# Kernel optimization log

Measured on AMD Instinct MI355X. Metric: run time of the kernel, lower is better.

## Reference

```python
import jax, jax.numpy as jnp
import numpy as np

TOP_K = 2  # MoE top-k routing


def setup_inputs() -> dict:
    key = jax.random.key(0)
    ks = jax.random.split(key, 5)
    B, D, H, O, N = 8192, 3072, 128, 10, 8
    scale_g = 1.0 / np.sqrt(D)
    return {
        "x": jax.random.normal(ks[0], (B, D), dtype=jnp.float32),
        "Wg": jax.random.normal(ks[1], (D, N), dtype=jnp.float32) * scale_g,
        "bg": jnp.zeros((N,), dtype=jnp.float32),
        "W1": jax.random.normal(ks[2], (N, D, H), dtype=jnp.float32) * scale_g,
        "b1": jnp.zeros((N, H), dtype=jnp.float32),
        "W2": jax.random.normal(ks[3], (N, H, O), dtype=jnp.float32) * (1.0 / np.sqrt(H)),
        "b2": jnp.zeros((N, O), dtype=jnp.float32),
    }


def reference(x, Wg, bg, W1, b1, W2, b2):
    # Gating: logits -> top-k -> softmax over the k selected logits
    g = x @ Wg + bg                                  # [B, N]
    tv, ti = jax.lax.top_k(g, TOP_K)                 # [B, k]
    w = jax.nn.softmax(tv, axis=-1)                  # [B, k]
    # Expert MLPs, computed densely over all experts (vectorized dispatch)
    h = jax.nn.relu(jnp.einsum('bd,edh->beh', x, W1) + b1)   # [B, N, H]
    y = jnp.einsum('beh,eho->beo', h, W2) + b2               # [B, N, O]
    # Combine: gather each token's k selected expert outputs, weight, sum
    ysel = jnp.take_along_axis(y, ti[:, :, None], axis=1)    # [B, k, O]
    return jnp.sum(w[:, :, None] * ysel, axis=1)             # [B, O]
```

## Files before the change

### kernel.cpp

```cpp
#include <hip/hip_runtime.h>
#include <hip/hip_bf16.h>

#define B_TOK 8192
#define D_DIM 3072
#define H_DIM 128
#define O_DIM 10
#define N_EXP 8

#define BM 128
#define BK2 128
#define HLDS_STRIDE 136

typedef __bf16 bf16x8 __attribute__((ext_vector_type(8)));
typedef float  f32x4  __attribute__((ext_vector_type(4)));
typedef unsigned short us8 __attribute__((ext_vector_type(8)));

__device__ __forceinline__ unsigned short f2bf(float f) {
  unsigned int u = __float_as_uint(f);
  unsigned int r = (u + 0x7FFFu + ((u >> 16) & 1u)) >> 16;
  return (unsigned short)r;
}

__device__ __forceinline__ void async16(const void* g, void* l) {
  __builtin_amdgcn_global_load_lds(
      (const __attribute__((address_space(1))) void*)g,
      (__attribute__((address_space(3))) void*)l,
      16, 0, 0);
}

__global__ __launch_bounds__(256) void k0_w1_transpose(const float* __restrict__ W1,
                                                       unsigned short* __restrict__ w1t) {
  __shared__ __align__(16) unsigned short lds[64 * 72];
  const int e  = blockIdx.z;
  const int d0 = blockIdx.x * 64;
  const int h0 = blockIdx.y * 64;
  const int tid = threadIdx.x;

  const float* src = W1 + ((size_t)e * D_DIM + d0) * H_DIM + h0;
  const int hl = tid & 63;
  const int dg = tid >> 6;
#pragma unroll
  for (int k = 0; k < 16; ++k) {
    const int d = dg + 4 * k;
    lds[hl * 72 + d] = f2bf(src[(size_t)d * H_DIM + hl]);
  }
  __syncthreads();

  unsigned short* dst = w1t + ((size_t)e * H_DIM + h0) * D_DIM + d0;
  const int q  = tid & 7;
  const int h1 = tid >> 3;
#pragma unroll
  for (int k = 0; k < 2; ++k) {
    const int h = h1 + 32 * k;
    const int d = q * 8;
    us8 v = *(const us8*)(lds + h * 72 + d);
    *(us8*)(dst + (size_t)h * D_DIM + d) = v;
  }
}

__global__ __launch_bounds__(512) void k1_gate_convert(
    const float* __restrict__ x, const float* __restrict__ Wg,
    const float* __restrict__ bg, unsigned short* __restrict__ xb,
    int4* __restrict__ idx4, float2* __restrict__ wts, int* __restrict__ cnt) {
  __shared__ float wg_lds[N_EXP * D_DIM];
  __shared__ int lcnt[N_EXP], gbase[N_EXP];
  const int tid = threadIdx.x;

  if (tid < N_EXP) lcnt[tid] = 0;
  for (int f = tid; f < D_DIM * N_EXP / 4; f += 512) {
    const float4 v = ((const float4*)Wg)[f];
    const int d  = f >> 1;
    const int nh = (f & 1) * 4;
    wg_lds[(nh + 0) * D_DIM + d] = v.x;
    wg_lds[(nh + 1) * D_DIM + d] = v.y;
    wg_lds[(nh + 2) * D_DIM + d] = v.z;
    wg_lds[(nh + 3) * D_DIM + d] = v.w;
  }
  __syncthreads();

  const int lane = tid & 63;
  const int wv   = tid >> 6;
  const int tk0  = blockIdx.x * 32 + wv * 4;

  const float* xr0 = x + (size_t)(tk0 + 0) * D_DIM;
  const float* xr1 = x + (size_t)(tk0 + 1) * D_DIM;
  const float* xr2 = x + (size_t)(tk0 + 2) * D_DIM;
  const float* xr3 = x + (size_t)(tk0 + 3) * D_DIM;
  unsigned short* xw0 = xb + (size_t)(tk0 + 0) * D_DIM;
  unsigned short* xw1 = xb + (size_t)(tk0 + 1) * D_DIM;
  unsigned short* xw2 = xb + (size_t)(tk0 + 2) * D_DIM;
  unsigned short* xw3 = xb + (size_t)(tk0 + 3) * D_DIM;

  float acc[4][N_EXP];
#pragma unroll
  for (int t = 0; t < 4; ++t)
#pragma unroll
    for (int n = 0; n < N_EXP; ++n) acc[t][n] = 0.f;

#pragma unroll 2
  for (int jj = 0; jj < D_DIM / 64; ++jj) {
    const int d = jj * 64 + lane;
    float w8[N_EXP];
#pragma unroll
    for (int n = 0; n < N_EXP; ++n) w8[n] = wg_lds[n * D_DIM + d];
    const float x0 = xr0[d], x1 = xr1[d], x2 = xr2[d], x3 = xr3[d];
    xw0[d] = f2bf(x0); xw1[d] = f2bf(x1); xw2[d] = f2bf(x2); xw3[d] = f2bf(x3);
#pragma unroll
    for (int n = 0; n < N_EXP; ++n) {
      acc[0][n] = fmaf(x0, w8[n], acc[0][n]);
      acc[1][n] = fmaf(x1, w8[n], acc[1][n]);
      acc[2][n] = fmaf(x2, w8[n], acc[2][n]);
      acc[3][n] = fmaf(x3, w8[n], acc[3][n]);
    }
  }

#pragma unroll
  for (int t = 0; t < 4; ++t)
#pragma unroll
    for (int n = 0; n < N_EXP; ++n) {
#pragma unroll
      for (int off = 32; off > 0; off >>= 1)
        acc[t][n] += __shfl_xor(acc[t][n], off, 64);
    }

  int li0[4], li1[4], lp0[4], lp1[4];
  float lw0[4], lw1[4];
  if (lane == 0) {
#pragma unroll
    for (int t = 0; t < 4; ++t) {
      float g[N_EXP];
#pragma unroll
      for (int n = 0; n < N_EXP; ++n) g[n] = acc[t][n] + bg[n];
      int i0 = 0;
#pragma unroll
      for (int n = 1; n < N_EXP; ++n) if (g[n] > g[i0]) i0 = n;
      int i1 = (i0 == 0) ? 1 : 0;
#pragma unroll
      for (int n = 0; n < N_EXP; ++n) if (n != i0 && g[n] > g[i1]) i1 = n;
      float e1 = expf(g[i1] - g[i0]);
      float inv = 1.f / (1.f + e1);
      li0[t] = i0; li1[t] = i1;
      lw0[t] = inv; lw1[t] = e1 * inv;
      lp0[t] = atomicAdd(&lcnt[i0], 1);
      lp1[t] = atomicAdd(&lcnt[i1], 1);
    }
  }
  __syncthreads();
  if (tid < N_EXP) gbase[tid] = atomicAdd(&cnt[tid], lcnt[tid]);
  __syncthreads();
  if (lane == 0) {
#pragma unroll
    for (int t = 0; t < 4; ++t) {
      idx4[tk0 + t] = make_int4(li0[t], gbase[li0[t]] + lp0[t],
                                li1[t], gbase[li1[t]] + lp1[t]);
      wts[tk0 + t]  = make_float2(lw0[t], lw1[t]);
    }
  }
}

__global__ void k1b1_scan(const int* __restrict__ cnt, int* __restrict__ off_g) {
  if (threadIdx.x == 0) {
    int s = 0;
#pragma unroll
    for (int n = 0; n < N_EXP; ++n) {
      off_g[n] = s;
      s += (cnt[n] + BM - 1) / BM * BM;
    }
    off_g[N_EXP] = s;
  }
}

__global__ __launch_bounds__(256) void k1b2_scatter(
    const int* __restrict__ off_g, const int4* __restrict__ idx4,
    int* __restrict__ tlist) {
  const int t = blockIdx.x * 256 + threadIdx.x;
  if (t >= B_TOK) return;
  const int4 r = idx4[t];
  tlist[off_g[r.x] + r.y] = t;
  tlist[off_g[r.z] + r.w] = t;
}

__global__ __launch_bounds__(256) void k2_experts(
    const unsigned short* __restrict__ xb,
    const unsigned short* __restrict__ w1t,
    const float* __restrict__ b1,
    const float* __restrict__ W2,
    const float* __restrict__ b2,
    const int* __restrict__ cnt, const int* __restrict__ off_g,
    const int* __restrict__ tlist,
    float* __restrict__ ypair) {
  const int e    = blockIdx.y;
  const int n_e  = cnt[e];
  const int row0 = blockIdx.x * BM;
  if (row0 >= n_e) return;
  const int off_e = off_g[e];

  __shared__ __align__(16) unsigned short sm[65536 + 2048];
  unsigned short* h_lds   = sm;
  unsigned short* w2t_lds = sm + 65536;

  const int tid  = threadIdx.x;
  const int lane = tid & 63;
  const int wv   = tid >> 6;

  const float* W2e = W2 + (size_t)e * H_DIM * O_DIM;
  for (int idx = tid; idx < 16 * 128; idx += 256) {
    int o = idx >> 7, hh = idx & 127;
    float v = (o < O_DIM) ? W2e[hh * O_DIM + o] : 0.f;
    w2t_lds[idx] = f2bf(v);
  }

  const int mhalf = (wv >> 1) * 64;
  const int nhalf = (wv & 1) * 64;

  f32x4 acc[4][4];
#pragma unroll
  for (int i = 0; i < 4; ++i)
#pragma unroll
    for (int j = 0; j < 4; ++j)
      acc[i][j] = (f32x4){0.f, 0.f, 0.f, 0.f};

  const int quad = lane >> 4;
  const int koff0 = (lane & 15) * 8;
  const unsigned short* Abase[8];
  const unsigned short* Bbase[8];
#pragma unroll
  for (int j = 0; j < 8; ++j) {
    int rloc = wv * 32 + j * 4 + quad;
    int gr = row0 + rloc;
    gr = gr < n_e ? gr : n_e - 1;
    Abase[j] = xb + (size_t)tlist[off_e + gr] * D_DIM + koff0;
    Bbase[j] = w1t + ((size_t)e * H_DIM + rloc) * D_DIM + koff0;
  }

#define STAGE(it, pp)                                                     \
  {                                                                       \
    const int ko = (it) * BK2;                                            \
    unsigned short* abuf = sm + (pp) * 32768;                             \
    unsigned short* bbuf = sm + 16384 + (pp) * 32768;                     \
    _Pragma("unroll")                                                     \
    for (int j = 0; j < 8; ++j) {                                         \
      const int ldsrow = (wv * 32 + j * 4) * BK2;                         \
      async16(Abase[j] + ko, abuf + ldsrow);                              \
      async16(Bbase[j] + ko, bbuf + ldsrow);                              \
    }                                                                     \
  }

  STAGE(0, 0);

  const int NIT = D_DIM / BK2;
  for (int it = 0; it < NIT; ++it) {
    __syncthreads();
    if (it + 1 < NIT) STAGE(it + 1, (it + 1) & 1);
    const unsigned short* al = sm + (it & 1) * 32768;
    const unsigned short* bl = sm + 16384 + (it & 1) * 32768;
#pragma unroll
    for (int kk = 0; kk < 4; ++kk) {
      const int krd = kk * 32 + quad * 8;
      bf16x8 af[4], bfr[4];
#pragma unroll
      for (int mi = 0; mi < 4; ++mi)
        af[mi] = *(const bf16x8*)(al + (mhalf + mi * 16 + (lane & 15)) * BK2 + krd);
#pragma unroll
      for (int ni = 0; ni < 4; ++ni)
        bfr[ni] = *(const bf16x8*)(bl + (nhalf + ni * 16 + (lane & 15)) * BK2 + krd);
#pragma unroll
      for (int mi = 0; mi < 4; ++mi)
#pragma unroll
        for (int ni = 0; ni < 4; ++ni)
          acc[mi][ni] = __builtin_amdgcn_mfma_f32_16x16x32_bf16(af[mi], bfr[ni], acc[mi][ni], 0, 0, 0);
    }
  }
  __syncthreads();

  const float* b1e = b1 + e * H_DIM;
#pragma unroll
  for (int ni = 0; ni < 4; ++ni) {
    const int col  = nhalf + ni * 16 + (lane & 15);
    const float bias = b1e[col];
#pragma unroll
    for (int mi = 0; mi < 4; ++mi) {
      const int rbase = mhalf + mi * 16 + (quad << 2);
#pragma unroll
      for (int r = 0; r < 4; ++r) {
        float v = acc[mi][ni][r] + bias;
        v = v > 0.f ? v : 0.f;
        h_lds[(rbase + r) * HLDS_STRIDE + col] = f2bf(v);
      }
    }
  }
  __syncthreads();

  f32x4 acc2[2];
  acc2[0] = (f32x4){0.f, 0.f, 0.f, 0.f};
  acc2[1] = (f32x4){0.f, 0.f, 0.f, 0.f};
#pragma unroll
  for (int ks = 0; ks < 4; ++ks) {
    const int krd = ks * 32 + quad * 8;
    bf16x8 bfr = *(const bf16x8*)(w2t_lds + (lane & 15) * 128 + krd);
#pragma unroll
    for (int mi = 0; mi < 2; ++mi) {
      bf16x8 afr = *(const bf16x8*)(h_lds + (wv * 32 + mi * 16 + (lane & 15)) * HLDS_STRIDE + krd);
      acc2[mi] = __builtin_amdgcn_mfma_f32_16x16x32_bf16(afr, bfr, acc2[mi], 0, 0, 0);
    }
  }
  const int o = lane & 15;
  if (o < O_DIM) {
    const float bias2 = b2[e * O_DIM + o];
#pragma unroll
    for (int mi = 0; mi < 2; ++mi) {
#pragma unroll
      for (int r = 0; r < 4; ++r) {
        const int rl = wv * 32 + mi * 16 + (quad << 2) + r;
        if (row0 + rl < n_e)
          ypair[(size_t)(off_e + row0 + rl) * 16 + o] = acc2[mi][r] + bias2;
      }
    }
  }
}

__global__ __launch_bounds__(256) void k3_combine(
    const float* __restrict__ ypair, const int4* __restrict__ idx4,
    const float2* __restrict__ wts, const int* __restrict__ off_g,
    float* __restrict__ out) {
  const int g = blockIdx.x * 256 + threadIdx.x;
  if (g >= B_TOK * O_DIM) return;
  const int b = g / O_DIM, o = g - b * O_DIM;
  const int4 r = idx4[b];
  const float2 w = wts[b];
  out[g] = w.x * ypair[(size_t)(off_g[r.x] + r.y) * 16 + o] +
           w.y * ypair[(size_t)(off_g[r.z] + r.w) * 16 + o];
}

extern "C" void kernel_launch(void* const* d_in, const int* in_sizes, int n_in,
                              void* d_out, int out_size, void* d_ws, size_t ws_size,
                              hipStream_t stream) {
  const float* x  = (const float*)d_in[0];
  const float* Wg = (const float*)d_in[1];
  const float* bg = (const float*)d_in[2];
  const float* W1 = (const float*)d_in[3];
  const float* b1 = (const float*)d_in[4];
  const float* W2 = (const float*)d_in[5];
  const float* b2 = (const float*)d_in[6];
  float* out = (float*)d_out;

  char* ws = (char*)d_ws;
  unsigned short* xb  = (unsigned short*)ws;
  unsigned short* w1t = (unsigned short*)(ws + 50331648);
  int4*   idx4  = (int4*)  (ws + 56623104);
  float2* wts   = (float2*)(ws + 56754176);
  int*    cnt   = (int*)   (ws + 56819712);
  int*    off_g = (int*)   (ws + 56819840);
  int*    tlist = (int*)   (ws + 56819968);
  float*  ypair = (float*) (ws + 56890112);

  k0_w1_transpose<<<dim3(48, 2, 8), dim3(256), 0, stream>>>(W1, w1t);
  (void)hipMemsetAsync(cnt, 0, N_EXP * sizeof(int), stream);
  k1_gate_convert<<<dim3(B_TOK / 32), dim3(512), 0, stream>>>(x, Wg, bg, xb, idx4, wts, cnt);
  k1b1_scan<<<dim3(1), dim3(64), 0, stream>>>(cnt, off_g);
  k1b2_scatter<<<dim3(B_TOK / 256), dim3(256), 0, stream>>>(off_g, idx4, tlist);
  k2_experts<<<dim3(B_TOK / BM, N_EXP), dim3(256), 0, stream>>>(
      xb, w1t, b1, W2, b2, cnt, off_g, tlist, ypair);
  k3_combine<<<dim3((B_TOK * O_DIM + 255) / 256), dim3(256), 0, stream>>>(
      ypair, idx4, wts, off_g, out);
}
```

Measured before the change: 270.6 us.

## Split gate GEMV over D chunks with separate top-k reduction kernel

The fused gate/convert kernel is split in two. The first kernel processes 768-wide D chunks across a 2D grid, using vectorized float4 loads of x and the gate weights, and writes per-chunk partial logits. The second kernel sums the four partials, adds the bias, and does top-2 selection, softmax and expert counting. This shrinks the LDS footprint per block and gives many more, smaller blocks, aiming for higher occupancy and bandwidth while streaming x. The cost is one extra launch and a small partial-logit buffer that aliases later workspace regions.

```diff
diff --git a/kernel.cpp b/kernel.cpp
--- a/kernel.cpp
+++ b/kernel.cpp
@@ -10,6 +10,8 @@
 #define BM 128
 #define BK2 128
 #define HLDS_STRIDE 136
+#define CHK 768
+#define NCHK 4
 
 typedef __bf16 bf16x8 __attribute__((ext_vector_type(8)));
 typedef float  f32x4  __attribute__((ext_vector_type(4)));
@@ -58,38 +60,37 @@
   }
 }
 
-__global__ __launch_bounds__(512) void k1_gate_convert(
+__global__ __launch_bounds__(256) void k1a_stream(
     const float* __restrict__ x, const float* __restrict__ Wg,
-    const float* __restrict__ bg, unsigned short* __restrict__ xb,
-    int4* __restrict__ idx4, float2* __restrict__ wts, int* __restrict__ cnt) {
-  __shared__ float wg_lds[N_EXP * D_DIM];
-  __shared__ int lcnt[N_EXP], gbase[N_EXP];
+    unsigned short* __restrict__ xb, float* __restrict__ gpart) {
+  __shared__ float wg_lds[N_EXP * CHK];
+  const int c   = blockIdx.y;
+  const int d0  = c * CHK;
   const int tid = threadIdx.x;
 
-  if (tid < N_EXP) lcnt[tid] = 0;
-  for (int f = tid; f < D_DIM * N_EXP / 4; f += 512) {
-    const float4 v = ((const float4*)Wg)[f];
-    const int d  = f >> 1;
+  for (int f = tid; f < CHK * N_EXP / 4; f += 256) {
+    const float4 v = ((const float4*)(Wg + (size_t)d0 * N_EXP))[f];
+    const int dl = f >> 1;
     const int nh = (f & 1) * 4;
-    wg_lds[(nh + 0) * D_DIM + d] = v.x;
-    wg_lds[(nh + 1) * D_DIM + d] = v.y;
-    wg_lds[(nh + 2) * D_DIM + d] = v.z;
-    wg_lds[(nh + 3) * D_DIM + d] = v.w;
+    wg_lds[(nh + 0) * CHK + dl] = v.x;
+    wg_lds[(nh + 1) * CHK + dl] = v.y;
+    wg_lds[(nh + 2) * CHK + dl] = v.z;
+    wg_lds[(nh + 3) * CHK + dl] = v.w;
   }
   __syncthreads();
 
   const int lane = tid & 63;
   const int wv   = tid >> 6;
-  const int tk0  = blockIdx.x * 32 + wv * 4;
-
-  const float* xr0 = x + (size_t)(tk0 + 0) * D_DIM;
-  const float* xr1 = x + (size_t)(tk0 + 1) * D_DIM;
-  const float* xr2 = x + (size_t)(tk0 + 2) * D_DIM;
-  const float* xr3 = x + (size_t)(tk0 + 3) * D_DIM;
-  unsigned short* xw0 = xb + (size_t)(tk0 + 0) * D_DIM;
-  unsigned short* xw1 = xb + (size_t)(tk0 + 1) * D_DIM;
-  unsigned short* xw2 = xb + (size_t)(tk0 + 2) * D_DIM;
-  unsigned short* xw3 = xb + (size_t)(tk0 + 3) * D_DIM;
+  const int t0   = blockIdx.x * 16 + wv * 4;
+
+  const float* xr0 = x + (size_t)(t0 + 0) * D_DIM + d0;
+  const float* xr1 = x + (size_t)(t0 + 1) * D_DIM + d0;
+  const float* xr2 = x + (size_t)(t0 + 2) * D_DIM + d0;
+  const float* xr3 = x + (size_t)(t0 + 3) * D_DIM + d0;
+  unsigned short* xw0 = xb + (size_t)(t0 + 0) * D_DIM + d0;
+  unsigned short* xw1 = xb + (size_t)(t0 + 1) * D_DIM + d0;
+  unsigned short* xw2 = xb + (size_t)(t0 + 2) * D_DIM + d0;
+  unsigned short* xw3 = xb + (size_t)(t0 + 3) * D_DIM + d0;
 
   float acc[4][N_EXP];
 #pragma unroll
@@ -97,20 +98,44 @@
 #pragma unroll
     for (int n = 0; n < N_EXP; ++n) acc[t][n] = 0.f;
 
-#pragma unroll 2
-  for (int jj = 0; jj < D_DIM / 64; ++jj) {
-    const int d = jj * 64 + lane;
-    float w8[N_EXP];
-#pragma unroll
-    for (int n = 0; n < N_EXP; ++n) w8[n] = wg_lds[n * D_DIM + d];
-    const float x0 = xr0[d], x1 = xr1[d], x2 = xr2[d], x3 = xr3[d];
-    xw0[d] = f2bf(x0); xw1[d] = f2bf(x1); xw2[d] = f2bf(x2); xw3[d] = f2bf(x3);
+#pragma unroll
+  for (int s = 0; s < CHK / 256; ++s) {
+    const int dl = s * 256 + lane * 4;
+    float4 xv0 = *(const float4*)(xr0 + dl);
+    float4 xv1 = *(const float4*)(xr1 + dl);
+    float4 xv2 = *(const float4*)(xr2 + dl);
+    float4 xv3 = *(const float4*)(xr3 + dl);
+    float4 w4[N_EXP];
+#pragma unroll
+    for (int n = 0; n < N_EXP; ++n)
+      w4[n] = *(const float4*)(wg_lds + n * CHK + dl);
+    ushort4 p;
+    p.x = f2bf(xv0.x); p.y = f2bf(xv0.y); p.z = f2bf(xv0.z); p.w = f2bf(xv0.w);
+    *(ushort4*)(xw0 + dl) = p;
+    p.x = f2bf(xv1.x); p.y = f2bf(xv1.y); p.z = f2bf(xv1.z); p.w = f2bf(xv1.w);
+    *(ushort4*)(xw1 + dl) = p;
+    p.x = f2bf(xv2.x); p.y = f2bf(xv2.y); p.z = f2bf(xv2.z); p.w = f2bf(xv2.w);
+    *(ushort4*)(xw2 + dl) = p;
+    p.x = f2bf(xv3.x); p.y = f2bf(xv3.y); p.z = f2bf(xv3.z); p.w = f2bf(xv3.w);
+    *(ushort4*)(xw3 + dl) = p;
 #pragma unroll
     for (int n = 0; n < N_EXP; ++n) {
-      acc[0][n] = fmaf(x0, w8[n], acc[0][n]);
-      acc[1][n] = fmaf(x1, w8[n], acc[1][n]);
-      acc[2][n] = fmaf(x2, w8[n], acc[2][n]);
-      acc[3][n] = fmaf(x3, w8[n], acc[3][n]);
+      acc[0][n] = fmaf(xv0.x, w4[n].x, acc[0][n]);
+      acc[0][n] = fmaf(xv0.y, w4[n].y, acc[0][n]);
+      acc[0][n] = fmaf(xv0.z, w4[n].z, acc[0][n]);
+      acc[0][n] = fmaf(xv0.w, w4[n].w, acc[0][n]);
+      acc[1][n] = fmaf(xv1.x, w4[n].x, acc[1][n]);
+      acc[1][n] = fmaf(xv1.y, w4[n].y, acc[1][n]);
+      acc[1][n] = fmaf(xv1.z, w4[n].z, acc[1][n]);
+      acc[1][n] = fmaf(xv1.w, w4[n].w, acc[1][n]);
+      acc[2][n] = fmaf(xv2.x, w4[n].x, acc[2][n]);
+      acc[2][n] = fmaf(xv2.y, w4[n].y, acc[2][n]);
+      acc[2][n] = fmaf(xv2.z, w4[n].z, acc[2][n]);
+      acc[2][n] = fmaf(xv2.w, w4[n].w, acc[2][n]);
+      acc[3][n] = fmaf(xv3.x, w4[n].x, acc[3][n]);
+      acc[3][n] = fmaf(xv3.y, w4[n].y, acc[3][n]);
+      acc[3][n] = fmaf(xv3.z, w4[n].z, acc[3][n]);
+      acc[3][n] = fmaf(xv3.w, w4[n].w, acc[3][n]);
     }
   }
 
@@ -122,40 +147,52 @@
       for (int off = 32; off > 0; off >>= 1)
         acc[t][n] += __shfl_xor(acc[t][n], off, 64);
     }
-
-  int li0[4], li1[4], lp0[4], lp1[4];
-  float lw0[4], lw1[4];
   if (lane == 0) {
 #pragma unroll
     for (int t = 0; t < 4; ++t) {
-      float g[N_EXP];
-#pragma unroll
-      for (int n = 0; n < N_EXP; ++n) g[n] = acc[t][n] + bg[n];
-      int i0 = 0;
-#pragma unroll
-      for (int n = 1; n < N_EXP; ++n) if (g[n] > g[i0]) i0 = n;
-      int i1 = (i0 == 0) ? 1 : 0;
-#pragma unroll
-      for (int n = 0; n < N_EXP; ++n) if (n != i0 && g[n] > g[i1]) i1 = n;
-      float e1 = expf(g[i1] - g[i0]);
-      float inv = 1.f / (1.f + e1);
-      li0[t] = i0; li1[t] = i1;
-      lw0[t] = inv; lw1[t] = e1 * inv;
-      lp0[t] = atomicAdd(&lcnt[i0], 1);
-      lp1[t] = atomicAdd(&lcnt[i1], 1);
-    }
-  }
+      float* gp = gpart + ((size_t)c * B_TOK + (t0 + t)) * N_EXP;
+      *(float4*)(gp)     = make_float4(acc[t][0], acc[t][1], acc[t][2], acc[t][3]);
+      *(float4*)(gp + 4) = make_float4(acc[t][4], acc[t][5], acc[t][6], acc[t][7]);
+    }
+  }
+}
+
+__global__ __launch_bounds__(256) void k1c_topk(
+    const float* __restrict__ gpart, const float* __restrict__ bg,
+    int4* __restrict__ idx4, float2* __restrict__ wts, int* __restrict__ cnt) {
+  __shared__ int lcnt[N_EXP], gbase[N_EXP];
+  __shared__ float bgs[N_EXP];
+  const int tid = threadIdx.x;
+  if (tid < N_EXP) { lcnt[tid] = 0; bgs[tid] = bg[tid]; }
+  __syncthreads();
+  const int t = blockIdx.x * 256 + tid;
+
+  float g[N_EXP];
+#pragma unroll
+  for (int n = 0; n < N_EXP; ++n) g[n] = bgs[n];
+#pragma unroll
+  for (int c = 0; c < NCHK; ++c) {
+    const float* gp = gpart + ((size_t)c * B_TOK + t) * N_EXP;
+    float4 a = *(const float4*)(gp);
+    float4 b = *(const float4*)(gp + 4);
+    g[0] += a.x; g[1] += a.y; g[2] += a.z; g[3] += a.w;
+    g[4] += b.x; g[5] += b.y; g[6] += b.z; g[7] += b.w;
+  }
+  int i0 = 0;
+#pragma unroll
+  for (int n = 1; n < N_EXP; ++n) if (g[n] > g[i0]) i0 = n;
+  int i1 = (i0 == 0) ? 1 : 0;
+#pragma unroll
+  for (int n = 0; n < N_EXP; ++n) if (n != i0 && g[n] > g[i1]) i1 = n;
+  const float e1 = expf(g[i1] - g[i0]);
+  const float inv = 1.f / (1.f + e1);
+  const int lp0 = atomicAdd(&lcnt[i0], 1);
+  const int lp1 = atomicAdd(&lcnt[i1], 1);
   __syncthreads();
   if (tid < N_EXP) gbase[tid] = atomicAdd(&cnt[tid], lcnt[tid]);
   __syncthreads();
-  if (lane == 0) {
-#pragma unroll
-    for (int t = 0; t < 4; ++t) {
-      idx4[tk0 + t] = make_int4(li0[t], gbase[li0[t]] + lp0[t],
-                                li1[t], gbase[li1[t]] + lp1[t]);
-      wts[tk0 + t]  = make_float2(lw0[t], lw1[t]);
-    }
-  }
+  idx4[t] = make_int4(i0, gbase[i0] + lp0, i1, gbase[i1] + lp1);
+  wts[t]  = make_float2(inv, e1 * inv);
 }
 
 __global__ void k1b1_scan(const int* __restrict__ cnt, int* __restrict__ off_g) {
@@ -351,12 +388,14 @@
   float2* wts   = (float2*)(ws + 56754176);
   int*    cnt   = (int*)   (ws + 56819712);
   int*    off_g = (int*)   (ws + 56819840);
-  int*    tlist = (int*)   (ws + 56819968);
-  float*  ypair = (float*) (ws + 56890112);
+  float*  gpart = (float*) (ws + 56890112);
+  int*    tlist = (int*)   (ws + 56890112);
+  float*  ypair = (float*) (ws + 56960256);
 
   k0_w1_transpose<<<dim3(48, 2, 8), dim3(256), 0, stream>>>(W1, w1t);
   (void)hipMemsetAsync(cnt, 0, N_EXP * sizeof(int), stream);
-  k1_gate_convert<<<dim3(B_TOK / 32), dim3(512), 0, stream>>>(x, Wg, bg, xb, idx4, wts, cnt);
+  k1a_stream<<<dim3(B_TOK / 16, NCHK), dim3(256), 0, stream>>>(x, Wg, xb, gpart);
+  k1c_topk<<<dim3(B_TOK / 256), dim3(256), 0, stream>>>(gpart, bg, idx4, wts, cnt);
   k1b1_scan<<<dim3(1), dim3(64), 0, stream>>>(cnt, off_g);
   k1b2_scatter<<<dim3(B_TOK / 256), dim3(256), 0, stream>>>(off_g, idx4, tlist);
   k2_experts<<<dim3(B_TOK / BM, N_EXP), dim3(256), 0, stream>>>(
```

Result: faster. 261.5 us (-3.4%).
